# Kernel tuning notes

Hardware: AMD Instinct MI355X
Metric: run time of the kernel (lower is better)

## Reference

```python
import jax, jax.numpy as jnp
import numpy as np

HS = 256      # hidden_size
HD = 256      # hidden_dim
B, L, S = 256, 400, 512
N = B * L
E = N * 4
NEG_SLOPE = 0.2


def setup_inputs() -> dict:
    key = jax.random.key(0)
    ks = iter(jax.random.split(key, 48))
    def rn(shape, scale=0.05):
        return jax.random.normal(next(ks), shape, jnp.float32) * scale
    inp = {}
    inp['emb'] = jax.random.normal(next(ks), (N, 640), jnp.float32)
    inp['x_tokens'] = jax.random.randint(next(ks), (N,), 0, 6, jnp.int32)
    inp['edge_src'] = jax.random.randint(next(ks), (E,), 0, N, jnp.int32)
    inp['edge_dst'] = jax.random.randint(next(ks), (E,), 0, N, jnp.int32)
    inp['batch_ids'] = (jnp.arange(N, dtype=jnp.int32) // L)
    inp['pos_ids'] = (jnp.arange(N, dtype=jnp.int32) % L)
    inp['mask'] = (jnp.arange(S)[None, :] < L).astype(jnp.float32) * jnp.ones((B, 1), jnp.float32)
    # parameters
    inp['emb_table'] = rn((6, HS))
    inp['W_e2g'] = rn((640, HS)); inp['b_e2g'] = jnp.zeros((HS,), jnp.float32)
    # GAT layers: (in, heads*out), att_src/att_dst [heads, out], bias [out]
    inp['W1'] = rn((HS, 4 * HD)); inp['asrc1'] = rn((4, HD)); inp['adst1'] = rn((4, HD)); inp['b1'] = jnp.zeros((HD,), jnp.float32)
    inp['W2'] = rn((HD, 4 * HD)); inp['asrc2'] = rn((4, HD)); inp['adst2'] = rn((4, HD)); inp['b2'] = jnp.zeros((HD,), jnp.float32)
    inp['W3'] = rn((HD, 1 * HS)); inp['asrc3'] = rn((1, HS)); inp['adst3'] = rn((1, HS)); inp['b3'] = jnp.zeros((HS,), jnp.float32)
    inp['W_le'] = rn((640, HS)); inp['b_le'] = jnp.zeros((HS,), jnp.float32)
    # CNN conv kernels: OIH layout [out=128, in=256, k]
    inp['k7'] = rn((HS // 2, HS, 7)); inp['cb7'] = jnp.zeros((HS // 2,), jnp.float32)
    inp['k11'] = rn((HS // 2, HS, 11)); inp['cb11'] = jnp.zeros((HS // 2,), jnp.float32)
    inp['k15'] = rn((HS // 2, HS, 15)); inp['cb15'] = jnp.zeros((HS // 2,), jnp.float32)
    inp['Wl1'] = rn((HS // 2, 512)); inp['bl1'] = jnp.zeros((512,), jnp.float32)
    inp['Wl2'] = rn((512, HS)); inp['bl2'] = jnp.zeros((HS,), jnp.float32)
    return inp


def _gat(x, src, dst, W, a_src, a_dst, b, heads, out_dim):
    # PyG GATConv, concat=False, eval (no dropout), with self-loops.
    n = x.shape[0]
    h = (x @ W).reshape(n, heads, out_dim)             # [N,H,C]
    al_s = (h * a_src[None]).sum(-1)                   # [N,H]
    al_d = (h * a_dst[None]).sum(-1)                   # [N,H]
    e = al_s[src] + al_d[dst]                          # [E,H]
    e = jnp.where(e > 0, e, NEG_SLOPE * e)             # leaky_relu(0.2)
    m = jax.ops.segment_max(e, dst, num_segments=n)
    m = jnp.where(jnp.isfinite(m), m, 0.0)
    ex = jnp.exp(e - m[dst])
    denom = jax.ops.segment_sum(ex, dst, num_segments=n) + 1e-16
    alpha = ex / denom[dst]                            # [E,H]
    out = jax.ops.segment_sum(alpha[:, :, None] * h[src], dst, num_segments=n)
    return out.mean(axis=1) + b                        # concat=False -> mean over heads


def _conv1d(x, w, b, pad):
    # x: [B,C,S], w: [O,I,k]
    y = jax.lax.conv_general_dilated(x, w, (1,), [(pad, pad)],
                                     dimension_numbers=('NCH', 'OIH', 'NCH'))
    return y + b[None, :, None]


def reference(emb, x_tokens, edge_src, edge_dst, batch_ids, pos_ids, mask,
              emb_table, W_e2g, b_e2g,
              W1, asrc1, adst1, b1, W2, asrc2, adst2, b2, W3, asrc3, adst3, b3,
              W_le, b_le, k7, cb7, k11, cb11, k15, cb15, Wl1, bl1, Wl2, bl2):
    n = emb.shape[0]
    # self-loops (PyG GATConv default)
    loops = jnp.arange(n, dtype=edge_src.dtype)
    src = jnp.concatenate([edge_src, loops])
    dst = jnp.concatenate([edge_dst, loops])

    x_r = emb_table[x_tokens]                          # [N,HS]
    x_g = jax.nn.relu(emb @ W_e2g + b_e2g)             # [N,HS]
    x = jax.nn.relu(_gat(x_g, src, dst, W1, asrc1, adst1, b1, 4, HD))
    x = jax.nn.relu(_gat(x, src, dst, W2, asrc2, adst2, b2, 4, HD))
    x = jax.nn.relu(_gat(x, src, dst, W3, asrc3, adst3, b3, 1, HS))

    emb_l = jax.nn.relu(emb @ W_le + b_le)             # [N,HS]

    # ragged -> padded [B,S,HS] via scatter (vectorized form of the python loop)
    zeros = jnp.zeros((mask.shape[0], S, HS), jnp.float32)
    out_r = zeros.at[batch_ids, pos_ids].set((x_r + emb_l) / 2)

    # CNN (eval: dropout = identity)
    xc = out_r.transpose(0, 2, 1)                      # [B,HS,S]
    x1 = _conv1d(xc, k7, cb7, 3)
    x2 = _conv1d(xc, k11, cb11, 5)
    x3 = _conv1d(xc, k15, cb15, 7)
    xc = ((x1 + x2 + x3) / 3).transpose(0, 2, 1)       # [B,S,128]
    xc = jax.nn.relu(xc @ Wl1 + bl1) @ Wl2 + bl2       # [B,S,HS]

    emb_seq = (xc * mask[:, :, None]).mean(axis=1)     # [B,HS]
    return emb_seq
```

## Files before the change

kernel.cpp:

```cpp
#include <hip/hip_runtime.h>

#define NNODES 102400
#define NBATCH 256
#define LSEQ   400
#define SPAD   416
#define HS     256
#define KDIM   640
#define OC     128
#define NTAP   15
#define H1     512
#define STILE  80
#define SROWS  94

typedef __attribute__((ext_vector_type(8))) short short8;
typedef __attribute__((ext_vector_type(4))) float floatx4;

__device__ inline unsigned short f2bf(float f) {
    unsigned u = __builtin_bit_cast(unsigned, f);
    unsigned r = (u + 0x7FFFu + ((u >> 16) & 1u)) >> 16;
    return (unsigned short)r;
}

__device__ inline void gld_lds16(const void* g, void* l) {
    __builtin_amdgcn_global_load_lds(
        (const __attribute__((address_space(1))) unsigned int*)g,
        (__attribute__((address_space(3))) unsigned int*)l, 16, 0, 0);
}

__global__ __launch_bounds__(256) void setup_all(
    const float* __restrict__ k7, const float* __restrict__ k11,
    const float* __restrict__ k15, const float* __restrict__ cb7,
    const float* __restrict__ cb11, const float* __restrict__ cb15,
    const float* __restrict__ W_le, const float* __restrict__ Wl1,
    unsigned short* __restrict__ Wpk, float* __restrict__ bc,
    unsigned short* __restrict__ Wle_pk, unsigned short* __restrict__ Wl1_pk,
    unsigned short* __restrict__ seq, float* __restrict__ A_acc)
{
    int bid = blockIdx.x, tid = threadIdx.x;
    if (bid < 512) {
        int idx = bid * 256 + tid;
        int b = idx >> 9, within = idx & 511;
        int rowi = within >> 5, c = within & 31;
        int srow = rowi < 8 ? rowi : 400 + rowi;
        ((uint4*)seq)[((size_t)b * SPAD + srow) * 32 + c] = make_uint4(0u, 0u, 0u, 0u);
    } else if (bid < 2432) {
        int idx = (bid - 512) * 256 + tid;
        int oc = idx & (OC - 1);
        int ic = (idx >> 7) & (HS - 1);
        int d  = idx / (OC * HS);
        float wv = k15[(oc * HS + ic) * 15 + d];
        int t11 = d - 2;
        if (t11 >= 0 && t11 < 11) wv += k11[(oc * HS + ic) * 11 + t11];
        int t7 = d - 4;
        if (t7 >= 0 && t7 < 7)   wv += k7[(oc * HS + ic) * 7 + t7];
        wv *= (1.0f / 3.0f);
        int kc = ic >> 6, ks = (ic >> 5) & 1, qq = (ic >> 3) & 3, j = ic & 7;
        int nt = oc >> 4, n = oc & 15;
        int pidx = ((((d * 4 + kc) * 2 + ks) * 8 + nt) * 64 + (qq * 16 + n)) * 8 + j;
        Wpk[pidx] = f2bf(wv);
        if (idx < OC) bc[idx] = (cb7[idx] + cb11[idx] + cb15[idx]) * (1.0f / 3.0f);
    } else if (bid < 3072) {
        int idx = (bid - 2432) * 256 + tid;
        int k = idx >> 8, col = idx & 255;
        int t = k >> 6, ks = (k >> 5) & 1, qq = (k >> 3) & 3, j = k & 7;
        int nt = col >> 4, n = col & 15;
        int pidx = (((t * 2 + ks) * 16 + nt) * 64 + (qq * 16 + n)) * 8 + j;
        Wle_pk[pidx] = f2bf(W_le[k * 256 + col]);
    } else if (bid < 3328) {
        int idx = (bid - 3072) * 256 + tid;
        int k = idx >> 9, col = idx & 511;
        int ks = k >> 5, qq = (k >> 3) & 3, j = k & 7;
        int jbb = col >> 7, nhnt = (col >> 4) & 7, n = col & 15;
        int pidx = jbb * 16384 + ((ks * 8 + nhnt) * 64 + (qq * 16 + n)) * 8 + j;
        Wl1_pk[pidx] = f2bf(Wl1[k * 512 + col]);
    } else {
        int idx = (bid - 3328) * 256 + tid;
        ((float4*)A_acc)[idx] = make_float4(0.f, 0.f, 0.f, 0.f);
    }
}

union GemmSm {
    unsigned short As[2][64][72];
    unsigned short Cs[64][264];
};

__global__ __launch_bounds__(256, 3) void gemm_emb(
    const float* __restrict__ emb, const int* __restrict__ x_tokens,
    const float* __restrict__ emb_table,
    const unsigned short* __restrict__ Wle_pk, const float* __restrict__ b_le,
    unsigned short* __restrict__ seq)
{
    __shared__ __align__(16) GemmSm g;
    int row0 = blockIdx.x * 64;
    int tid = threadIdx.x;
    int w = tid >> 6, lane = tid & 63;
    int q = lane >> 4, m = lane & 15;

    int ar = tid >> 2;
    int ac = (tid & 3) * 16;

    const short8* wle = (const short8*)Wle_pk;
    const float4* arow = (const float4*)&emb[(size_t)(row0 + ar) * KDIM + ac];

    float4 aregA[4], aregB[4];
    #pragma unroll
    for (int u = 0; u < 4; u++) aregA[u] = arow[u];
    #pragma unroll
    for (int u = 0; u < 4; u++) aregB[u] = arow[16 + u];
    #pragma unroll
    for (int u = 0; u < 4; u++) {
        float4 f = aregA[u];
        ushort4 h; h.x = f2bf(f.x); h.y = f2bf(f.y); h.z = f2bf(f.z); h.w = f2bf(f.w);
        *(ushort4*)&g.As[0][ar][ac + u * 4] = h;
    }
    asm volatile("s_waitcnt lgkmcnt(0)" ::: "memory");
    __builtin_amdgcn_s_barrier();

    floatx4 acc[4][4] = {};
    for (int tt = 0; tt < 10; tt += 2) {
        {
            const int t = tt;
            short8 bf[8];
            #pragma unroll
            for (int ks = 0; ks < 2; ks++)
                #pragma unroll
                for (int nt = 0; nt < 4; nt++)
                    bf[ks * 4 + nt] = wle[(size_t)t * 2048 + ks * 1024 + (w * 4 + nt) * 64 + lane];
            if (t + 2 < 10) {
                #pragma unroll
                for (int u = 0; u < 4; u++) aregA[u] = arow[(t + 2) * 16 + u];
            }
            #pragma unroll
            for (int ks = 0; ks < 2; ks++) {
                #pragma unroll
                for (int mt = 0; mt < 4; mt++) {
                    short8 a = *(const short8*)&g.As[0][mt * 16 + m][ks * 32 + q * 8];
                    #pragma unroll
                    for (int nt = 0; nt < 4; nt++)
                        acc[mt][nt] = __builtin_amdgcn_mfma_f32_16x16x32_bf16(a, bf[ks * 4 + nt], acc[mt][nt], 0, 0, 0);
                }
            }
            if (t + 1 < 10) {
                #pragma unroll
                for (int u = 0; u < 4; u++) {
                    float4 f = aregB[u];
                    ushort4 h; h.x = f2bf(f.x); h.y = f2bf(f.y); h.z = f2bf(f.z); h.w = f2bf(f.w);
                    *(ushort4*)&g.As[1][ar][ac + u * 4] = h;
                }
            }
            asm volatile("s_waitcnt lgkmcnt(0)" ::: "memory");
            __builtin_amdgcn_s_barrier();
        }
        {
            const int t = tt + 1;
            short8 bf[8];
            #pragma unroll
            for (int ks = 0; ks < 2; ks++)
                #pragma unroll
                for (int nt = 0; nt < 4; nt++)
                    bf[ks * 4 + nt] = wle[(size_t)t * 2048 + ks * 1024 + (w * 4 + nt) * 64 + lane];
            if (t + 2 < 10) {
                #pragma unroll
                for (int u = 0; u < 4; u++) aregB[u] = arow[(t + 2) * 16 + u];
            }
            #pragma unroll
            for (int ks = 0; ks < 2; ks++) {
                #pragma unroll
                for (int mt = 0; mt < 4; mt++) {
                    short8 a = *(const short8*)&g.As[1][mt * 16 + m][ks * 32 + q * 8];
                    #pragma unroll
                    for (int nt = 0; nt < 4; nt++)
                        acc[mt][nt] = __builtin_amdgcn_mfma_f32_16x16x32_bf16(a, bf[ks * 4 + nt], acc[mt][nt], 0, 0, 0);
                }
            }
            if (t + 1 < 10) {
                #pragma unroll
                for (int u = 0; u < 4; u++) {
                    float4 f = aregA[u];
                    ushort4 h; h.x = f2bf(f.x); h.y = f2bf(f.y); h.z = f2bf(f.z); h.w = f2bf(f.w);
                    *(ushort4*)&g.As[0][ar][ac + u * 4] = h;
                }
            }
            asm volatile("s_waitcnt lgkmcnt(0)" ::: "memory");
            __builtin_amdgcn_s_barrier();
        }
    }

    #pragma unroll
    for (int nt = 0; nt < 4; nt++) {
        int col = w * 64 + nt * 16 + m;
        float blv = b_le[col];
        #pragma unroll
        for (int mt = 0; mt < 4; mt++) {
            #pragma unroll
            for (int r = 0; r < 4; r++) {
                int row = mt * 16 + q * 4 + r;
                int tok = x_tokens[row0 + row];
                float v = acc[mt][nt][r] + blv;
                v = v > 0.f ? v : 0.f;
                g.Cs[row][col] = f2bf(0.5f * (v + emb_table[tok * HS + col]));
            }
        }
    }
    asm volatile("s_waitcnt lgkmcnt(0)" ::: "memory");
    __builtin_amdgcn_s_barrier();
    #pragma unroll
    for (int rr = 0; rr < 16; rr++) {
        int node = row0 + w * 16 + rr;
        int b = node / LSEQ;
        int p = node - b * LSEQ;
        ushort4 val = *(const ushort4*)&g.Cs[w * 16 + rr][lane * 4];
        *(ushort4*)&seq[((size_t)b * SPAD + (p + 8)) * HS + lane * 4] = val;
    }
}

union ConvSm {
    unsigned short As[SROWS][264];
    struct {
        float red[40 * 132];
        unsigned short abf[STILE][136];
    } p2;
};

__device__ __forceinline__ void conv_load_Bh(
    const short8* __restrict__ wb, int h, int kh, int nh, int lane, short8 bf[4])
{
    int c = h >> 1, ks = h & 1;
    int d = c >> 1, kc = kh * 2 + (c & 1);
    const short8* bp = wb + (size_t)(d * 4 + kc) * 1024 + nh * 256 + ks * 512 + lane;
    #pragma unroll
    for (int nt = 0; nt < 4; nt++)
        bf[nt] = bp[nt * 64];
}

__device__ __forceinline__ void conv_mfma_half(
    const unsigned short (*As)[264], floatx4 acc[5][4],
    const short8 bf[4], int h, int kh, int m, int q)
{
    int c = h >> 1, ks = h & 1;
    int d = c >> 1, kc = kh * 2 + (c & 1);
    #pragma unroll
    for (int mt = 0; mt < 5; mt++) {
        short8 a = *(const short8*)&As[mt * 16 + m + d][kc * 64 + ks * 32 + q * 8];
        #pragma unroll
        for (int nt = 0; nt < 4; nt++)
            acc[mt][nt] = __builtin_amdgcn_mfma_f32_16x16x32_bf16(a, bf[nt], acc[mt][nt], 0, 0, 0);
    }
}

__global__ __launch_bounds__(256, 3) void conv_fused(
    const unsigned short* __restrict__ seq, const unsigned short* __restrict__ Wpk,
    const float* __restrict__ bc, const unsigned short* __restrict__ Wl1_pk,
    const float* __restrict__ bl1, float* __restrict__ A_acc)
{
    __shared__ __align__(16) ConvSm sm;

    int b  = blockIdx.y;
    int s0 = blockIdx.x * STILE;
    int tid = threadIdx.x;
    int w = tid >> 6, lane = tid & 63;
    int q = lane >> 4, m = lane & 15;
    int nh = w >> 1, kh = w & 1;

    const short8* wb = (const short8*)Wpk;
    short8 bA[4], bB[4];
    conv_load_Bh(wb, 0, kh, nh, lane, bA);

    {
        const uint4* sp = (const uint4*)(seq + ((size_t)b * SPAD + s0 + 1) * HS);
        #pragma unroll
        for (int pass = 0; pass < 12; pass++) {
            int idx = pass * 256 + tid;
            if (idx < SROWS * 32) {
                int r = idx >> 5, c = idx & 31;
                *(uint4*)&sm.As[r][c * 8] = sp[r * 32 + c];
            }
        }
    }
    __syncthreads();

    floatx4 acc[5][4] = {};

    for (int h = 0; h < 60; h += 2) {
        conv_load_Bh(wb, h + 1, kh, nh, lane, bB);
        conv_mfma_half(sm.As, acc, bA, h, kh, m, q);
        if (h + 2 < 60) conv_load_Bh(wb, h + 2, kh, nh, lane, bA);
        conv_mfma_half(sm.As, acc, bB, h + 1, kh, m, q);
    }

    float bc0 = bc[lane * 2], bc1 = bc[lane * 2 + 1];
    __syncthreads();
    #pragma unroll
    for (int hh = 0; hh < 2; hh++) {
        if (kh == 1) {
            #pragma unroll
            for (int mt = 0; mt < 5; mt++)
                #pragma unroll
                for (int nt = 0; nt < 4; nt++)
                    #pragma unroll
                    for (int r = 0; r < 4; r++) {
                        int row = mt * 16 + q * 4 + r;
                        if (row >= hh * 40 && row < hh * 40 + 40)
                            sm.p2.red[(row - hh * 40) * 132 + nh * 64 + nt * 16 + m] = acc[mt][nt][r];
                    }
        }
        __syncthreads();
        if (kh == 0) {
            #pragma unroll
            for (int mt = 0; mt < 5; mt++)
                #pragma unroll
                for (int nt = 0; nt < 4; nt++)
                    #pragma unroll
                    for (int r = 0; r < 4; r++) {
                        int row = mt * 16 + q * 4 + r;
                        if (row >= hh * 40 && row < hh * 40 + 40)
                            sm.p2.red[(row - hh * 40) * 132 + nh * 64 + nt * 16 + m] += acc[mt][nt][r];
                    }
        }
        __syncthreads();
        #pragma unroll
        for (int rr = 0; rr < 10; rr++) {
            int lrow = w * 10 + rr;
            float2 v = *(const float2*)&sm.p2.red[lrow * 132 + lane * 2];
            unsigned uo = (unsigned)f2bf(v.x + bc0) | ((unsigned)f2bf(v.y + bc1) << 16);
            *(unsigned*)&sm.p2.abf[hh * 40 + lrow][lane * 2] = uo;
        }
        __syncthreads();
    }

    const short8* wl1 = (const short8*)Wl1_pk;
    short8 f0[8], f1[8];
    #pragma unroll
    for (int ks = 0; ks < 4; ks++)
        #pragma unroll
        for (int nt = 0; nt < 2; nt++)
            f0[ks * 2 + nt] = wl1[(ks * 8 + w * 2 + nt) * 64 + lane];
    #pragma unroll
    for (int ks = 0; ks < 4; ks++)
        #pragma unroll
        for (int nt = 0; nt < 2; nt++)
            f1[ks * 2 + nt] = wl1[2048 + (ks * 8 + w * 2 + nt) * 64 + lane];

    #pragma unroll
    for (int jb = 0; jb < 4; jb++) {
        floatx4 acc2[5][2] = {};
        const short8* fcur = (jb & 1) ? f1 : f0;
        #pragma unroll
        for (int ks = 0; ks < 4; ks++) {
            short8 bf0 = fcur[ks * 2 + 0];
            short8 bf1 = fcur[ks * 2 + 1];
            #pragma unroll
            for (int mt = 0; mt < 5; mt++) {
                short8 a = *(const short8*)&sm.p2.abf[mt * 16 + m][ks * 32 + q * 8];
                acc2[mt][0] = __builtin_amdgcn_mfma_f32_16x16x32_bf16(a, bf0, acc2[mt][0], 0, 0, 0);
                acc2[mt][1] = __builtin_amdgcn_mfma_f32_16x16x32_bf16(a, bf1, acc2[mt][1], 0, 0, 0);
            }
        }
        if (jb < 2) {
            short8* fnext = (jb & 1) ? f1 : f0;
            #pragma unroll
            for (int ks = 0; ks < 4; ks++)
                #pragma unroll
                for (int nt = 0; nt < 2; nt++)
                    fnext[ks * 2 + nt] = wl1[(size_t)(jb + 2) * 2048 + (ks * 8 + w * 2 + nt) * 64 + lane];
        }
        #pragma unroll
        for (int nt = 0; nt < 2; nt++) {
            int j = jb * 128 + w * 32 + nt * 16 + m;
            float blv = bl1[j];
            float vsum = 0.f;
            #pragma unroll
            for (int mt = 0; mt < 5; mt++)
                #pragma unroll
                for (int r = 0; r < 4; r++) {
                    float v = acc2[mt][nt][r] + blv;
                    vsum += v > 0.f ? v : 0.f;
                }
            vsum += __shfl_xor(vsum, 16, 64);
            vsum += __shfl_xor(vsum, 32, 64);
            if (q == 0) atomicAdd(&A_acc[(size_t)b * H1 + j], vsum);
        }
    }
}

__global__ __launch_bounds__(256) void final_out(
    const float* __restrict__ A_acc, const float* __restrict__ Wl2,
    const float* __restrict__ bl2, float* __restrict__ out)
{
    __shared__ float a[H1];
    int b = blockIdx.x, tid = threadIdx.x;
    a[tid] = A_acc[(size_t)b * H1 + tid];
    a[tid + 256] = A_acc[(size_t)b * H1 + tid + 256];
    __syncthreads();
    float acc = 0.f;
    #pragma unroll 8
    for (int k = 0; k < H1; k++)
        acc += a[k] * Wl2[(size_t)k * HS + tid];
    out[(size_t)b * HS + tid] = acc * (1.0f / 512.0f) + bl2[tid] * (400.0f / 512.0f);
}

extern "C" void kernel_launch(void* const* d_in, const int* in_sizes, int n_in,
                              void* d_out, int out_size, void* d_ws, size_t ws_size,
                              hipStream_t stream)
{
    const float* emb       = (const float*)d_in[0];
    const int*   x_tokens  = (const int*)d_in[1];
    const float* emb_table = (const float*)d_in[7];
    const float* W_le = (const float*)d_in[22];
    const float* b_le = (const float*)d_in[23];
    const float* k7   = (const float*)d_in[24];
    const float* cb7  = (const float*)d_in[25];
    const float* k11  = (const float*)d_in[26];
    const float* cb11 = (const float*)d_in[27];
    const float* k15  = (const float*)d_in[28];
    const float* cb15 = (const float*)d_in[29];
    const float* Wl1  = (const float*)d_in[30];
    const float* bl1  = (const float*)d_in[31];
    const float* Wl2  = (const float*)d_in[32];
    const float* bl2  = (const float*)d_in[33];
    float* out = (float*)d_out;

    char* p = (char*)d_ws;
    unsigned short* seqb = (unsigned short*)p;       p += (size_t)NBATCH * SPAD * HS * 2;
    unsigned short* Wpk = (unsigned short*)p;        p += (size_t)NTAP * HS * OC * 2;
    unsigned short* Wle_pk = (unsigned short*)p;     p += (size_t)KDIM * HS * 2;
    unsigned short* Wl1_pk = (unsigned short*)p;     p += (size_t)OC * H1 * 2;
    float* bcv = (float*)p;                          p += 512;
    float* A_acc = (float*)p;                        p += (size_t)NBATCH * H1 * 4;

    setup_all<<<dim3(3456), 256, 0, stream>>>(
        k7, k11, k15, cb7, cb11, cb15, W_le, Wl1,
        Wpk, bcv, Wle_pk, Wl1_pk, seqb, A_acc);
    gemm_emb<<<dim3(NNODES / 64), 256, 0, stream>>>(
        emb, x_tokens, emb_table, Wle_pk, b_le, seqb);
    conv_fused<<<dim3(5, NBATCH), 256, 0, stream>>>(
        seqb, Wpk, bcv, Wl1_pk, bl1, A_acc);
    final_out<<<NBATCH, 256, 0, stream>>>(A_acc, Wl2, bl2, out);
}
```

Before: 578.8 us.

## Fuse embedding GEMM into conv kernel, recomputing halo rows per tile

Merges the embedding projection GEMM into the conv kernel. Each block now computes its own 96-row slice of emb@W_le plus the token embedding, with zeros at the sequence edges, straight into shared memory. This removes the padded bf16 sequence buffer, its global write and read, its zero-initialisation and one kernel launch. In exchange, the 16 halo rows are recomputed by neighbouring tiles, which adds GEMM work and re-reads part of emb. Shared memory and register use also grow, so occupancy is lowered to 2 blocks per CU.

```diff
diff --git a/kernel.cpp b/kernel.cpp
--- a/kernel.cpp
+++ b/kernel.cpp
@@ -3,14 +3,13 @@
 #define NNODES 102400
 #define NBATCH 256
 #define LSEQ   400
-#define SPAD   416
 #define HS     256
 #define KDIM   640
 #define OC     128
 #define NTAP   15
 #define H1     512
 #define STILE  80
-#define SROWS  94
+#define GR     96
 
 typedef __attribute__((ext_vector_type(8))) short short8;
 typedef __attribute__((ext_vector_type(4))) float floatx4;
@@ -19,12 +18,6 @@
     unsigned u = __builtin_bit_cast(unsigned, f);
     unsigned r = (u + 0x7FFFu + ((u >> 16) & 1u)) >> 16;
     return (unsigned short)r;
-}
-
-__device__ inline void gld_lds16(const void* g, void* l) {
-    __builtin_amdgcn_global_load_lds(
-        (const __attribute__((address_space(1))) unsigned int*)g,
-        (__attribute__((address_space(3))) unsigned int*)l, 16, 0, 0);
 }
 
 __global__ __launch_bounds__(256) void setup_all(
@@ -34,17 +27,11 @@
     const float* __restrict__ W_le, const float* __restrict__ Wl1,
     unsigned short* __restrict__ Wpk, float* __restrict__ bc,
     unsigned short* __restrict__ Wle_pk, unsigned short* __restrict__ Wl1_pk,
-    unsigned short* __restrict__ seq, float* __restrict__ A_acc)
+    float* __restrict__ A_acc)
 {
     int bid = blockIdx.x, tid = threadIdx.x;
-    if (bid < 512) {
+    if (bid < 1920) {
         int idx = bid * 256 + tid;
-        int b = idx >> 9, within = idx & 511;
-        int rowi = within >> 5, c = within & 31;
-        int srow = rowi < 8 ? rowi : 400 + rowi;
-        ((uint4*)seq)[((size_t)b * SPAD + srow) * 32 + c] = make_uint4(0u, 0u, 0u, 0u);
-    } else if (bid < 2432) {
-        int idx = (bid - 512) * 256 + tid;
         int oc = idx & (OC - 1);
         int ic = (idx >> 7) & (HS - 1);
         int d  = idx / (OC * HS);
@@ -59,163 +46,31 @@
         int pidx = ((((d * 4 + kc) * 2 + ks) * 8 + nt) * 64 + (qq * 16 + n)) * 8 + j;
         Wpk[pidx] = f2bf(wv);
         if (idx < OC) bc[idx] = (cb7[idx] + cb11[idx] + cb15[idx]) * (1.0f / 3.0f);
-    } else if (bid < 3072) {
-        int idx = (bid - 2432) * 256 + tid;
+    } else if (bid < 2560) {
+        int idx = (bid - 1920) * 256 + tid;
         int k = idx >> 8, col = idx & 255;
         int t = k >> 6, ks = (k >> 5) & 1, qq = (k >> 3) & 3, j = k & 7;
         int nt = col >> 4, n = col & 15;
         int pidx = (((t * 2 + ks) * 16 + nt) * 64 + (qq * 16 + n)) * 8 + j;
         Wle_pk[pidx] = f2bf(W_le[k * 256 + col]);
-    } else if (bid < 3328) {
-        int idx = (bid - 3072) * 256 + tid;
+    } else if (bid < 2816) {
+        int idx = (bid - 2560) * 256 + tid;
         int k = idx >> 9, col = idx & 511;
         int ks = k >> 5, qq = (k >> 3) & 3, j = k & 7;
         int jbb = col >> 7, nhnt = (col >> 4) & 7, n = col & 15;
         int pidx = jbb * 16384 + ((ks * 8 + nhnt) * 64 + (qq * 16 + n)) * 8 + j;
         Wl1_pk[pidx] = f2bf(Wl1[k * 512 + col]);
     } else {
-        int idx = (bid - 3328) * 256 + tid;
+        int idx = (bid - 2816) * 256 + tid;
         ((float4*)A_acc)[idx] = make_float4(0.f, 0.f, 0.f, 0.f);
     }
 }
 
-union GemmSm {
-    unsigned short As[2][64][72];
-    unsigned short Cs[64][264];
-};
-
-__global__ __launch_bounds__(256, 3) void gemm_emb(
-    const float* __restrict__ emb, const int* __restrict__ x_tokens,
-    const float* __restrict__ emb_table,
-    const unsigned short* __restrict__ Wle_pk, const float* __restrict__ b_le,
-    unsigned short* __restrict__ seq)
-{
-    __shared__ __align__(16) GemmSm g;
-    int row0 = blockIdx.x * 64;
-    int tid = threadIdx.x;
-    int w = tid >> 6, lane = tid & 63;
-    int q = lane >> 4, m = lane & 15;
-
-    int ar = tid >> 2;
-    int ac = (tid & 3) * 16;
-
-    const short8* wle = (const short8*)Wle_pk;
-    const float4* arow = (const float4*)&emb[(size_t)(row0 + ar) * KDIM + ac];
-
-    float4 aregA[4], aregB[4];
-    #pragma unroll
-    for (int u = 0; u < 4; u++) aregA[u] = arow[u];
-    #pragma unroll
-    for (int u = 0; u < 4; u++) aregB[u] = arow[16 + u];
-    #pragma unroll
-    for (int u = 0; u < 4; u++) {
-        float4 f = aregA[u];
-        ushort4 h; h.x = f2bf(f.x); h.y = f2bf(f.y); h.z = f2bf(f.z); h.w = f2bf(f.w);
-        *(ushort4*)&g.As[0][ar][ac + u * 4] = h;
-    }
-    asm volatile("s_waitcnt lgkmcnt(0)" ::: "memory");
-    __builtin_amdgcn_s_barrier();
-
-    floatx4 acc[4][4] = {};
-    for (int tt = 0; tt < 10; tt += 2) {
-        {
-            const int t = tt;
-            short8 bf[8];
-            #pragma unroll
-            for (int ks = 0; ks < 2; ks++)
-                #pragma unroll
-                for (int nt = 0; nt < 4; nt++)
-                    bf[ks * 4 + nt] = wle[(size_t)t * 2048 + ks * 1024 + (w * 4 + nt) * 64 + lane];
-            if (t + 2 < 10) {
-                #pragma unroll
-                for (int u = 0; u < 4; u++) aregA[u] = arow[(t + 2) * 16 + u];
-            }
-            #pragma unroll
-            for (int ks = 0; ks < 2; ks++) {
-                #pragma unroll
-                for (int mt = 0; mt < 4; mt++) {
-                    short8 a = *(const short8*)&g.As[0][mt * 16 + m][ks * 32 + q * 8];
-                    #pragma unroll
-                    for (int nt = 0; nt < 4; nt++)
-                        acc[mt][nt] = __builtin_amdgcn_mfma_f32_16x16x32_bf16(a, bf[ks * 4 + nt], acc[mt][nt], 0, 0, 0);
-                }
-            }
-            if (t + 1 < 10) {
-                #pragma unroll
-                for (int u = 0; u < 4; u++) {
-                    float4 f = aregB[u];
-                    ushort4 h; h.x = f2bf(f.x); h.y = f2bf(f.y); h.z = f2bf(f.z); h.w = f2bf(f.w);
-                    *(ushort4*)&g.As[1][ar][ac + u * 4] = h;
-                }
-            }
-            asm volatile("s_waitcnt lgkmcnt(0)" ::: "memory");
-            __builtin_amdgcn_s_barrier();
-        }
-        {
-            const int t = tt + 1;
-            short8 bf[8];
-            #pragma unroll
-            for (int ks = 0; ks < 2; ks++)
-                #pragma unroll
-                for (int nt = 0; nt < 4; nt++)
-                    bf[ks * 4 + nt] = wle[(size_t)t * 2048 + ks * 1024 + (w * 4 + nt) * 64 + lane];
-            if (t + 2 < 10) {
-                #pragma unroll
-                for (int u = 0; u < 4; u++) aregB[u] = arow[(t + 2) * 16 + u];
-            }
-            #pragma unroll
-            for (int ks = 0; ks < 2; ks++) {
-                #pragma unroll
-                for (int mt = 0; mt < 4; mt++) {
-                    short8 a = *(const short8*)&g.As[1][mt * 16 + m][ks * 32 + q * 8];
-                    #pragma unroll
-                    for (int nt = 0; nt < 4; nt++)
-                        acc[mt][nt] = __builtin_amdgcn_mfma_f32_16x16x32_bf16(a, bf[ks * 4 + nt], acc[mt][nt], 0, 0, 0);
-                }
-            }
-            if (t + 1 < 10) {
-                #pragma unroll
-                for (int u = 0; u < 4; u++) {
-                    float4 f = aregA[u];
-                    ushort4 h; h.x = f2bf(f.x); h.y = f2bf(f.y); h.z = f2bf(f.z); h.w = f2bf(f.w);
-                    *(ushort4*)&g.As[0][ar][ac + u * 4] = h;
-                }
-            }
-            asm volatile("s_waitcnt lgkmcnt(0)" ::: "memory");
-            __builtin_amdgcn_s_barrier();
-        }
-    }
-
-    #pragma unroll
-    for (int nt = 0; nt < 4; nt++) {
-        int col = w * 64 + nt * 16 + m;
-        float blv = b_le[col];
-        #pragma unroll
-        for (int mt = 0; mt < 4; mt++) {
-            #pragma unroll
-            for (int r = 0; r < 4; r++) {
-                int row = mt * 16 + q * 4 + r;
-                int tok = x_tokens[row0 + row];
-                float v = acc[mt][nt][r] + blv;
-                v = v > 0.f ? v : 0.f;
-                g.Cs[row][col] = f2bf(0.5f * (v + emb_table[tok * HS + col]));
-            }
-        }
-    }
-    asm volatile("s_waitcnt lgkmcnt(0)" ::: "memory");
-    __builtin_amdgcn_s_barrier();
-    #pragma unroll
-    for (int rr = 0; rr < 16; rr++) {
-        int node = row0 + w * 16 + rr;
-        int b = node / LSEQ;
-        int p = node - b * LSEQ;
-        ushort4 val = *(const ushort4*)&g.Cs[w * 16 + rr][lane * 4];
-        *(ushort4*)&seq[((size_t)b * SPAD + (p + 8)) * HS + lane * 4] = val;
-    }
-}
-
-union ConvSm {
-    unsigned short As[SROWS][264];
+union FusedSm {
+    struct {
+        unsigned short As[GR][268];
+        unsigned short Ag[2][GR][76];
+    } g;
     struct {
         float red[40 * 132];
         unsigned short abf[STILE][136];
@@ -225,8 +80,8 @@
 __device__ __forceinline__ void conv_load_Bh(
     const short8* __restrict__ wb, int h, int kh, int nh, int lane, short8 bf[4])
 {
-    int c = h >> 1, ks = h & 1;
-    int d = c >> 1, kc = kh * 2 + (c & 1);
+    int cc = h >> 1, ks = h & 1;
+    int d = cc >> 1, kc = kh * 2 + (cc & 1);
     const short8* bp = wb + (size_t)(d * 4 + kc) * 1024 + nh * 256 + ks * 512 + lane;
     #pragma unroll
     for (int nt = 0; nt < 4; nt++)
@@ -234,11 +89,11 @@
 }
 
 __device__ __forceinline__ void conv_mfma_half(
-    const unsigned short (*As)[264], floatx4 acc[5][4],
+    const unsigned short (*As)[268], floatx4 acc[5][4],
     const short8 bf[4], int h, int kh, int m, int q)
 {
-    int c = h >> 1, ks = h & 1;
-    int d = c >> 1, kc = kh * 2 + (c & 1);
+    int cc = h >> 1, ks = h & 1;
+    int d = cc >> 1, kc = kh * 2 + (cc & 1);
     #pragma unroll
     for (int mt = 0; mt < 5; mt++) {
         short8 a = *(const short8*)&As[mt * 16 + m + d][kc * 64 + ks * 32 + q * 8];
@@ -248,44 +103,179 @@
     }
 }
 
-__global__ __launch_bounds__(256, 3) void conv_fused(
-    const unsigned short* __restrict__ seq, const unsigned short* __restrict__ Wpk,
-    const float* __restrict__ bc, const unsigned short* __restrict__ Wl1_pk,
-    const float* __restrict__ bl1, float* __restrict__ A_acc)
-{
-    __shared__ __align__(16) ConvSm sm;
+__global__ __launch_bounds__(256, 2) void fused_main(
+    const float* __restrict__ emb, const int* __restrict__ x_tokens,
+    const float* __restrict__ emb_table,
+    const unsigned short* __restrict__ Wle_pk, const float* __restrict__ b_le,
+    const unsigned short* __restrict__ Wpk, const float* __restrict__ bc,
+    const unsigned short* __restrict__ Wl1_pk, const float* __restrict__ bl1,
+    float* __restrict__ A_acc)
+{
+    __shared__ __align__(16) FusedSm sm;
 
     int b  = blockIdx.y;
     int s0 = blockIdx.x * STILE;
     int tid = threadIdx.x;
     int w = tid >> 6, lane = tid & 63;
     int q = lane >> 4, m = lane & 15;
+
+    int br = tid >> 4;
+    int c  = tid & 15;
+    const float4* pA[6];
+    bool vld[6];
+    #pragma unroll
+    for (int u = 0; u < 6; u++) {
+        int p = s0 - 7 + br + 16 * u;
+        vld[u] = (p >= 0) && (p < LSEQ);
+        int safe = vld[u] ? p : 0;
+        pA[u] = (const float4*)&emb[(size_t)(b * LSEQ + safe) * KDIM];
+    }
+
+    const short8* wle = (const short8*)Wle_pk;
+    float4 fA[6], fB[6];
+    #pragma unroll
+    for (int u = 0; u < 6; u++) fA[u] = pA[u][c];
+    #pragma unroll
+    for (int u = 0; u < 6; u++) fB[u] = pA[u][16 + c];
+    #pragma unroll
+    for (int u = 0; u < 6; u++) {
+        float4 f = fA[u];
+        ushort4 h;
+        h.x = vld[u] ? f2bf(f.x) : (unsigned short)0;
+        h.y = vld[u] ? f2bf(f.y) : (unsigned short)0;
+        h.z = vld[u] ? f2bf(f.z) : (unsigned short)0;
+        h.w = vld[u] ? f2bf(f.w) : (unsigned short)0;
+        *(ushort4*)&sm.g.Ag[0][br + 16 * u][c * 4] = h;
+    }
+    asm volatile("s_waitcnt lgkmcnt(0)" ::: "memory");
+    __builtin_amdgcn_s_barrier();
+
+    floatx4 acc[6][4] = {};
+    for (int tt = 0; tt < 10; tt += 2) {
+        {
+            const int t = tt;
+            short8 bf[8];
+            #pragma unroll
+            for (int ks = 0; ks < 2; ks++)
+                #pragma unroll
+                for (int nt = 0; nt < 4; nt++)
+                    bf[ks * 4 + nt] = wle[(size_t)t * 2048 + ks * 1024 + (w * 4 + nt) * 64 + lane];
+            if (t + 2 < 10) {
+                #pragma unroll
+                for (int u = 0; u < 6; u++) fA[u] = pA[u][(t + 2) * 16 + c];
+            }
+            #pragma unroll
+            for (int ks = 0; ks < 2; ks++) {
+                short8 a0 = *(const short8*)&sm.g.Ag[0][ 0 + m][ks * 32 + q * 8];
+                short8 a1 = *(const short8*)&sm.g.Ag[0][16 + m][ks * 32 + q * 8];
+                short8 a2 = *(const short8*)&sm.g.Ag[0][32 + m][ks * 32 + q * 8];
+                short8 a3 = *(const short8*)&sm.g.Ag[0][48 + m][ks * 32 + q * 8];
+                short8 a4 = *(const short8*)&sm.g.Ag[0][64 + m][ks * 32 + q * 8];
+                short8 a5 = *(const short8*)&sm.g.Ag[0][80 + m][ks * 32 + q * 8];
+                #pragma unroll
+                for (int nt = 0; nt < 4; nt++) {
+                    short8 bv = bf[ks * 4 + nt];
+                    acc[0][nt] = __builtin_amdgcn_mfma_f32_16x16x32_bf16(a0, bv, acc[0][nt], 0, 0, 0);
+                    acc[1][nt] = __builtin_amdgcn_mfma_f32_16x16x32_bf16(a1, bv, acc[1][nt], 0, 0, 0);
+                    acc[2][nt] = __builtin_amdgcn_mfma_f32_16x16x32_bf16(a2, bv, acc[2][nt], 0, 0, 0);
+                    acc[3][nt] = __builtin_amdgcn_mfma_f32_16x16x32_bf16(a3, bv, acc[3][nt], 0, 0, 0);
+                    acc[4][nt] = __builtin_amdgcn_mfma_f32_16x16x32_bf16(a4, bv, acc[4][nt], 0, 0, 0);
+                    acc[5][nt] = __builtin_amdgcn_mfma_f32_16x16x32_bf16(a5, bv, acc[5][nt], 0, 0, 0);
+                }
+            }
+            if (t + 1 < 10) {
+                #pragma unroll
+                for (int u = 0; u < 6; u++) {
+                    float4 f = fB[u];
+                    ushort4 h;
+                    h.x = vld[u] ? f2bf(f.x) : (unsigned short)0;
+                    h.y = vld[u] ? f2bf(f.y) : (unsigned short)0;
+                    h.z = vld[u] ? f2bf(f.z) : (unsigned short)0;
+                    h.w = vld[u] ? f2bf(f.w) : (unsigned short)0;
+                    *(ushort4*)&sm.g.Ag[1][br + 16 * u][c * 4] = h;
+                }
+            }
+            asm volatile("s_waitcnt lgkmcnt(0)" ::: "memory");
+            __builtin_amdgcn_s_barrier();
+        }
+        {
+            const int t = tt + 1;
+            short8 bf[8];
+            #pragma unroll
+            for (int ks = 0; ks < 2; ks++)
+                #pragma unroll
+                for (int nt = 0; nt < 4; nt++)
+                    bf[ks * 4 + nt] = wle[(size_t)t * 2048 + ks * 1024 + (w * 4 + nt) * 64 + lane];
+            if (t + 2 < 10) {
+                #pragma unroll
+                for (int u = 0; u < 6; u++) fB[u] = pA[u][(t + 2) * 16 + c];
+            }
+            #pragma unroll
+            for (int ks = 0; ks < 2; ks++) {
+                short8 a0 = *(const short8*)&sm.g.Ag[1][ 0 + m][ks * 32 + q * 8];
+                short8 a1 = *(const short8*)&sm.g.Ag[1][16 + m][ks * 32 + q * 8];
+                short8 a2 = *(const short8*)&sm.g.Ag[1][32 + m][ks * 32 + q * 8];
+                short8 a3 = *(const short8*)&sm.g.Ag[1][48 + m][ks * 32 + q * 8];
+                short8 a4 = *(const short8*)&sm.g.Ag[1][64 + m][ks * 32 + q * 8];
+                short8 a5 = *(const short8*)&sm.g.Ag[1][80 + m][ks * 32 + q * 8];
+                #pragma unroll
+                for (int nt = 0; nt < 4; nt++) {
+                    short8 bv = bf[ks * 4 + nt];
+                    acc[0][nt] = __builtin_amdgcn_mfma_f32_16x16x32_bf16(a0, bv, acc[0][nt], 0, 0, 0);
+                    acc[1][nt] = __builtin_amdgcn_mfma_f32_16x16x32_bf16(a1, bv, acc[1][nt], 0, 0, 0);
+                    acc[2][nt] = __builtin_amdgcn_mfma_f32_16x16x32_bf16(a2, bv, acc[2][nt], 0, 0, 0);
+                    acc[3][nt] = __builtin_amdgcn_mfma_f32_16x16x32_bf16(a3, bv, acc[3][nt], 0, 0, 0);
+                    acc[4][nt] = __builtin_amdgcn_mfma_f32_16x16x32_bf16(a4, bv, acc[4][nt], 0, 0, 0);
+                    acc[5][nt] = __builtin_amdgcn_mfma_f32_16x16x32_bf16(a5, bv, acc[5][nt], 0, 0, 0);
+                }
+            }
+            if (t + 1 < 10) {
+                #pragma unroll
+                for (int u = 0; u < 6; u++) {
+                    float4 f = fA[u];
+                    ushort4 h;
+                    h.x = vld[u] ? f2bf(f.x) : (unsigned short)0;
+                    h.y = vld[u] ? f2bf(f.y) : (unsigned short)0;
+                    h.z = vld[u] ? f2bf(f.z) : (unsigned short)0;
+                    h.w = vld[u] ? f2bf(f.w) : (unsigned short)0;
+                    *(ushort4*)&sm.g.Ag[0][br + 16 * u][c * 4] = h;
+                }
+            }
+            asm volatile("s_waitcnt lgkmcnt(0)" ::: "memory");
+            __builtin_amdgcn_s_barrier();
+        }
+    }
+
+    #pragma unroll
+    for (int mt = 0; mt < 6; mt++) {
+        #pragma unroll
+        for (int r = 0; r < 4; r++) {
+            int row = mt * 16 + q * 4 + r;
+            int p = s0 - 7 + row;
+            bool v = (p >= 0) && (p < LSEQ);
+            int tokb = v ? (x_tokens[b * LSEQ + p] * HS) : 0;
+            #pragma unroll
+            for (int nt = 0; nt < 4; nt++) {
+                int col = w * 64 + nt * 16 + m;
+                float vv = acc[mt][nt][r] + b_le[col];
+                vv = vv > 0.f ? vv : 0.f;
+                vv = 0.5f * (vv + emb_table[tokb + col]);
+                sm.g.As[row][col] = v ? f2bf(vv) : (unsigned short)0;
+            }
+        }
+    }
     int nh = w >> 1, kh = w & 1;
-
     const short8* wb = (const short8*)Wpk;
     short8 bA[4], bB[4];
     conv_load_Bh(wb, 0, kh, nh, lane, bA);
-
-    {
-        const uint4* sp = (const uint4*)(seq + ((size_t)b * SPAD + s0 + 1) * HS);
-        #pragma unroll
-        for (int pass = 0; pass < 12; pass++) {
-            int idx = pass * 256 + tid;
-            if (idx < SROWS * 32) {
-                int r = idx >> 5, c = idx & 31;
-                *(uint4*)&sm.As[r][c * 8] = sp[r * 32 + c];
-            }
-        }
-    }
     __syncthreads();
 
-    floatx4 acc[5][4] = {};
-
+    floatx4 acc3[5][4] = {};
     for (int h = 0; h < 60; h += 2) {
         conv_load_Bh(wb, h + 1, kh, nh, lane, bB);
-        conv_mfma_half(sm.As, acc, bA, h, kh, m, q);
+        conv_mfma_half(sm.g.As, acc3, bA, h, kh, m, q);
         if (h + 2 < 60) conv_load_Bh(wb, h + 2, kh, nh, lane, bA);
-        conv_mfma_half(sm.As, acc, bB, h + 1, kh, m, q);
+        conv_mfma_half(sm.g.As, acc3, bB, h + 1, kh, m, q);
     }
 
     float bc0 = bc[lane * 2], bc1 = bc[lane * 2 + 1];
@@ -301,7 +291,7 @@
                     for (int r = 0; r < 4; r++) {
                         int row = mt * 16 + q * 4 + r;
                         if (row >= hh * 40 && row < hh * 40 + 40)
-                            sm.p2.red[(row - hh * 40) * 132 + nh * 64 + nt * 16 + m] = acc[mt][nt][r];
+                            sm.p2.red[(row - hh * 40) * 132 + nh * 64 + nt * 16 + m] = acc3[mt][nt][r];
                     }
         }
         __syncthreads();
@@ -314,7 +304,7 @@
                     for (int r = 0; r < 4; r++) {
                         int row = mt * 16 + q * 4 + r;
                         if (row >= hh * 40 && row < hh * 40 + 40)
-                            sm.p2.red[(row - hh * 40) * 132 + nh * 64 + nt * 16 + m] += acc[mt][nt][r];
+                            sm.p2.red[(row - hh * 40) * 132 + nh * 64 + nt * 16 + m] += acc3[mt][nt][r];
                     }
         }
         __syncthreads();
@@ -421,19 +411,16 @@
     float* out = (float*)d_out;
 
     char* p = (char*)d_ws;
-    unsigned short* seqb = (unsigned short*)p;       p += (size_t)NBATCH * SPAD * HS * 2;
     unsigned short* Wpk = (unsigned short*)p;        p += (size_t)NTAP * HS * OC * 2;
     unsigned short* Wle_pk = (unsigned short*)p;     p += (size_t)KDIM * HS * 2;
     unsigned short* Wl1_pk = (unsigned short*)p;     p += (size_t)OC * H1 * 2;
     float* bcv = (float*)p;                          p += 512;
     float* A_acc = (float*)p;                        p += (size_t)NBATCH * H1 * 4;
 
-    setup_all<<<dim3(3456), 256, 0, stream>>>(
+    setup_all<<<dim3(2944), 256, 0, stream>>>(
         k7, k11, k15, cb7, cb11, cb15, W_le, Wl1,
-        Wpk, bcv, Wle_pk, Wl1_pk, seqb, A_acc);
-    gemm_emb<<<dim3(NNODES / 64), 256, 0, stream>>>(
-        emb, x_tokens, emb_table, Wle_pk, b_le, seqb);
-    conv_fused<<<dim3(5, NBATCH), 256, 0, stream>>>(
-        seqb, Wpk, bcv, Wl1_pk, bl1, A_acc);
+        Wpk, bcv, Wle_pk, Wl1_pk, A_acc);
+    fused_main<<<dim3(5, NBATCH), 256, 0, stream>>>(
+        emb, x_tokens, emb_table, Wle_pk, b_le, Wpk, bcv, Wl1_pk, bl1, A_acc);
     final_out<<<NBATCH, 256, 0, stream>>>(A_acc, Wl2, bl2, out);
 }
```

Result: slower. 740.7 us (+28.0%).
